# Kernel optimization log

Hardware: AMD Instinct MI355X
Metric: run time of the kernel (lower is better)

The kernel has to match this reference:

```python
import jax, jax.numpy as jnp
import numpy as np

EMBED = 256; G = 8; NC = 6; NL = 4; NP = 13
BS = 1; NA = 900
IMG_W, IMG_H = 704.0, 256.0
LEVEL_HW = [(64, 176), (32, 88), (16, 44), (8, 22)]


def setup_inputs() -> dict:
    key = jax.random.key(0)
    ks = jax.random.split(key, 12)
    inp = {}
    inp["instance_feature"] = jax.random.normal(ks[0], (BS, NA, EMBED), jnp.float32)
    inp["anchor_embed"] = jax.random.normal(ks[1], (BS, NA, EMBED), jnp.float32)
    # key points in normalized [0,1) cube; projection matrix maps them to pixel coords
    inp["key_points"] = jax.random.uniform(ks[2], (BS, NA, NP, 3), jnp.float32)
    for i, (h, w) in enumerate(LEVEL_HW):
        inp[f"fm{i}"] = jax.random.normal(ks[3 + i], (BS, NC, EMBED, h, w), jnp.float32)
    # intrinsics-like projection: x->x*W, y->y*H, depth ~ z+0.5, plus per-camera jitter
    base = jnp.array([[IMG_W, 0.0, 0.0, 0.0],
                      [0.0, IMG_H, 0.0, 0.0],
                      [0.0, 0.0, 1.0, 0.5],
                      [0.0, 0.0, 0.0, 1.0]], jnp.float32)
    inp["projection_mat"] = base[None, None] + 0.05 * jax.random.normal(ks[7], (BS, NC, 4, 4), jnp.float32)
    inp["image_wh"] = jnp.broadcast_to(jnp.array([IMG_W, IMG_H], jnp.float32), (BS, NC, 2))
    inp["w_weights"] = 0.02 * jax.random.normal(ks[8], (EMBED, G * NC * NL * NP), jnp.float32)
    inp["b_weights"] = jnp.zeros((G * NC * NL * NP,), jnp.float32)
    inp["w_out"] = 0.02 * jax.random.normal(ks[9], (EMBED, EMBED), jnp.float32)
    inp["b_out"] = jnp.zeros((EMBED,), jnp.float32)
    return inp


def _grid_sample(fm, grid):
    # fm: (B, C, H, W); grid: (B, A, P, 2) in [-1,1]. Bilinear, zero padding,
    # align_corners=False (torch F.grid_sample defaults). Returns (B, A, P, C).
    B, C, H, W = fm.shape
    A, P = grid.shape[1], grid.shape[2]
    gx = (grid[..., 0] + 1.0) * (W * 0.5) - 0.5
    gy = (grid[..., 1] + 1.0) * (H * 0.5) - 0.5
    x0 = jnp.floor(gx); y0 = jnp.floor(gy)
    fmf = jnp.transpose(fm.reshape(B, C, H * W), (0, 2, 1))  # (B, HW, C)

    def gather(xi, yi):
        valid = (xi >= 0) & (xi <= W - 1) & (yi >= 0) & (yi <= H - 1)
        xc = jnp.clip(xi, 0, W - 1).astype(jnp.int32)
        yc = jnp.clip(yi, 0, H - 1).astype(jnp.int32)
        idx = (yc * W + xc).reshape(B, A * P, 1)
        g = jnp.take_along_axis(fmf, idx, axis=1).reshape(B, A, P, C)
        return g * valid[..., None].astype(fm.dtype)

    wx1 = gx - x0; wx0 = 1.0 - wx1
    wy1 = gy - y0; wy0 = 1.0 - wy1
    return (gather(x0, y0) * (wx0 * wy0)[..., None]
            + gather(x0 + 1.0, y0) * (wx1 * wy0)[..., None]
            + gather(x0, y0 + 1.0) * (wx0 * wy1)[..., None]
            + gather(x0 + 1.0, y0 + 1.0) * (wx1 * wy1)[..., None])


def reference(instance_feature, anchor_embed, key_points, fm0, fm1, fm2, fm3,
              projection_mat, image_wh, w_weights, b_weights, w_out, b_out):
    bs, na = instance_feature.shape[:2]
    gd = EMBED // G
    # _get_weights: softmax over (cams*levels*pts) jointly, per group
    feat = instance_feature + anchor_embed
    w = (feat @ w_weights + b_weights).reshape(bs, na, NC * NL * NP, G)
    w = jax.nn.softmax(w, axis=2).reshape(bs, na, NC, NL, NP, G)
    # feature_sampling: project 3D key points to each camera's pixel plane
    kp_h = jnp.concatenate([key_points, jnp.ones_like(key_points[..., :1])], axis=-1)
    p2 = jnp.einsum('bcij,banj->bcani', projection_mat, kp_h)  # (bs,cams,na,pts,4)
    xy = p2[..., :2] / jnp.maximum(p2[..., 2:3], 1e-5)
    grid = (xy / image_wh[:, :, None, None]) * 2.0 - 1.0
    grid = grid.reshape(bs * NC, na, NP, 2)
    # bilinear sample every pyramid level for every camera
    feats = jnp.stack([
        _grid_sample(fm.reshape(bs * NC, EMBED, fm.shape[-2], fm.shape[-1]), grid)
        for fm in (fm0, fm1, fm2, fm3)
    ], axis=0)  # (L, bs*cams, na, pts, E)
    feats = feats.reshape(NL, bs, NC, na, NP, G, gd)
    # multi_view_level_fusion: weighted sum over cams and levels, per group
    fused = jnp.einsum('baclpg,lbcapgd->bapgd', w, feats).reshape(bs, na, NP, EMBED)
    out = fused.sum(axis=2)  # sum over key points
    return out @ w_out + b_out + instance_feature  # output_proj + residual 'add'
```

## Files before the change

kernel.cpp:

```cpp
#include <hip/hip_runtime.h>
#include <hip/hip_bf16.h>
#include <hip/hip_fp16.h>
#include <cstdint>

#define EMBED 256
#define GPS 8
#define NCAM 6
#define NLVL 4
#define NPT 13
#define NANC 900
#define NSAMP (NCAM*NLVL*NPT)
#define NWCOL (GPS*NSAMP)
#define MPAD 928
#define WSTRIDE 328

typedef __attribute__((ext_vector_type(8))) short bf16x8;
typedef __attribute__((ext_vector_type(16))) float f32x16;
typedef __attribute__((ext_vector_type(8))) unsigned short ushort8_t;

__device__ __forceinline__ ushort bf16bits(float x) {
    __hip_bfloat16 h = __float2bfloat16(x);
    return *reinterpret_cast<ushort*>(&h);
}
__device__ __forceinline__ ushort h16bits(float x) {
    __half h = __float2half(x);
    return *reinterpret_cast<ushort*>(&h);
}
__device__ __forceinline__ __half2 u2h2(unsigned u) {
    union { unsigned u; __half2 h; } cv; cv.u = u; return cv.h;
}

__global__ __launch_bounds__(256) void k_prep(
        const float* __restrict__ fm0, const float* __restrict__ fm1,
        const float* __restrict__ fm2, const float* __restrict__ fm3,
        __half* __restrict__ t0, __half* __restrict__ t1,
        __half* __restrict__ t2, __half* __restrict__ t3,
        const float* __restrict__ wlin, __hip_bfloat16* __restrict__ wt,
        const float* __restrict__ inst, const float* __restrict__ anch,
        __hip_bfloat16* __restrict__ featB,
        const float* __restrict__ kp, const float* __restrict__ proj,
        float* __restrict__ pxy) {
    __shared__ ushort lds2[256 * 64];
    int b = blockIdx.x;
    int t = threadIdx.x;
    if (b < 1404) {
        const float* in; __half* outp; int HW, chunks, lb;
        if (b < 1056)      { in = fm0; outp = t0; HW = 11264; chunks = 176; lb = b; }
        else if (b < 1320) { in = fm1; outp = t1; HW = 2816;  chunks = 44;  lb = b - 1056; }
        else if (b < 1386) { in = fm2; outp = t2; HW = 704;   chunks = 11;  lb = b - 1320; }
        else               { in = fm3; outp = t3; HW = 176;   chunks = 3;   lb = b - 1386; }
        int c = lb / chunks;
        int hw0 = (lb - c * chunks) * 64;
        int q = t & 15, eg = t >> 4;
        bool vld = (hw0 + q * 4 + 3) < HW;
        const float* srcq = in + (size_t)c * EMBED * HW + hw0 + q * 4;
        float4 vals[16];
        #pragma unroll
        for (int r = 0; r < 16; r++) {
            int e = eg + r * 16;
            vals[r] = vld ? *(const float4*)(srcq + (size_t)e * HW)
                          : make_float4(0.f, 0.f, 0.f, 0.f);
        }
        #pragma unroll
        for (int r = 0; r < 16; r++) {
            int e = eg + r * 16;
            int sw = ((e >> 3) & 15) * 4;
            ushort4 u;
            u.x = h16bits(vals[r].x); u.y = h16bits(vals[r].y);
            u.z = h16bits(vals[r].z); u.w = h16bits(vals[r].w);
            *reinterpret_cast<ushort4*>(&lds2[e * 64 + ((q * 4) ^ sw)]) = u;
        }
        __syncthreads();
        ushort* outb = reinterpret_cast<ushort*>(outp) + ((size_t)c * HW + hw0) * EMBED;
        #pragma unroll
        for (int r = 0; r < 8; r++) {
            int flat = r * 2048 + t * 8;
            int hw = flat >> 8;
            int e0 = flat & 255;
            if (hw0 + hw < HW) {
                ushort8_t u;
                #pragma unroll
                for (int j = 0; j < 8; j++) {
                    int e = e0 + j;
                    int sw = ((e >> 3) & 15) * 4;
                    u[j] = lds2[e * 64 + (hw ^ sw)];
                }
                *reinterpret_cast<ushort8_t*>(outb + flat) = u;
            }
        }
    } else if (b < 1560) {
        int b1 = b - 1404;
        int kt = b1 / 39, nt = b1 - kt * 39;
        int k0 = kt * 64, n0 = nt * 64;
        int grp = t >> 6, nn = t & 63;
        #pragma unroll
        for (int r = 0; r < 16; r++) {
            int kk = grp * 16 + r;
            lds2[kk * 65 + nn] = bf16bits(wlin[(size_t)(k0 + kk) * NWCOL + n0 + nn]);
        }
        __syncthreads();
        ushort* wtb = reinterpret_cast<ushort*>(wt);
        int kk2 = t & 63;
        #pragma unroll
        for (int r = 0; r < 16; r++) {
            int nn2 = grp * 16 + r;
            wtb[(size_t)(n0 + nn2) * EMBED + k0 + kk2] = lds2[kk2 * 65 + nn2];
        }
    } else if (b < 1785) {
        int base = (b - 1560) * 1024 + t * 4;
        float4 a = *(const float4*)&inst[base];
        float4 c = *(const float4*)&anch[base];
        ushort4 r;
        r.x = bf16bits(a.x + c.x); r.y = bf16bits(a.y + c.y);
        r.z = bf16bits(a.z + c.z); r.w = bf16bits(a.w + c.w);
        *reinterpret_cast<ushort4*>(reinterpret_cast<ushort*>(featB) + base) = r;
    } else if (b < 1792) {
        int base = 900 * EMBED + (b - 1785) * 1024 + t * 4;
        ushort4 z; z.x = z.y = z.z = z.w = 0;
        *reinterpret_cast<ushort4*>(reinterpret_cast<ushort*>(featB) + base) = z;
    } else {
        int i = (b - 1792) * 256 + t;
        if (i < NANC * NCAM * NPT) {
            int a = i / (NCAM * NPT);
            int r = i - a * (NCAM * NPT);
            int c = r / NPT;
            int p = r - c * NPT;
            const float* M = proj + c * 16;
            const float* k3 = kp + ((size_t)a * NPT + p) * 3;
            float kx = k3[0], ky = k3[1], kz = k3[2];
            float X = M[0] * kx + M[1] * ky + M[2] * kz + M[3];
            float Y = M[4] * kx + M[5] * ky + M[6] * kz + M[7];
            float Z = M[8] * kx + M[9] * ky + M[10] * kz + M[11];
            float invz = 1.f / fmaxf(Z, 1e-5f);
            pxy[(size_t)i * 2 + 0] = X * invz;
            pxy[(size_t)i * 2 + 1] = Y * invz;
        }
    }
}

#define MT 29
#define NT 78
__global__ __launch_bounds__(256) void k_gemm(const __hip_bfloat16* __restrict__ featB,
                                              const __hip_bfloat16* __restrict__ wt,
                                              const float* __restrict__ blin,
                                              float* __restrict__ logits) {
    int wv = threadIdx.x >> 6, lane = threadIdx.x & 63;
    int idx = blockIdx.x * 4 + wv;
    if (idx >= MT * NT) return;
    int mt = idx % MT, nt = idx / MT;
    int m0 = mt * 32, n0 = nt * 32;
    int l31 = lane & 31;
    int khalf = (lane >> 5) * 8;
    const short* ap = reinterpret_cast<const short*>(featB) + (size_t)(m0 + l31) * EMBED + khalf;
    const short* bp = reinterpret_cast<const short*>(wt)    + (size_t)(n0 + l31) * EMBED + khalf;
    f32x16 acc = {};
    #pragma unroll 8
    for (int ki = 0; ki < 16; ki++) {
        bf16x8 a = *reinterpret_cast<const bf16x8*>(ap + ki * 16);
        bf16x8 bb = *reinterpret_cast<const bf16x8*>(bp + ki * 16);
        acc = __builtin_amdgcn_mfma_f32_32x32x16_bf16(a, bb, acc, 0, 0, 0);
    }
    float bias = blin[n0 + l31];
    int colg = n0 + l31;
    #pragma unroll
    for (int r = 0; r < 16; r++) {
        int row = (r & 3) + 8 * (r >> 2) + 4 * (lane >> 5);
        int grow = m0 + row;
        if (grow < NANC)
            logits[(size_t)grow * NWCOL + colg] = acc[r] + bias;
    }
}

__global__ __launch_bounds__(512) void k_aggregate(const __half* __restrict__ f0,
                                                   const __half* __restrict__ f1,
                                                   const __half* __restrict__ f2,
                                                   const __half* __restrict__ f3,
                                                   const float* __restrict__ logits,
                                                   const float* __restrict__ pxy,
                                                   const float* __restrict__ wout,
                                                   const float* __restrict__ bout,
                                                   const float* __restrict__ inst,
                                                   float* __restrict__ out) {
    __shared__ float wT[GPS * WSTRIDE];
    __shared__ float xyS[NCAM * NPT * 2];
    __shared__ float redS[8][EMBED];
    __shared__ float pS[EMBED];
    int a = blockIdx.x;
    int tid = threadIdx.x;
    for (int j = tid; j < NWCOL; j += 512)
        wT[(j & 7) * WSTRIDE + (j >> 3)] = logits[(size_t)a * NWCOL + j];
    for (int j = tid; j < NCAM * NPT * 2; j += 512)
        xyS[j] = pxy[(size_t)a * NCAM * NPT * 2 + j];
    __syncthreads();
    int wave = tid >> 6;
    int lane = tid & 63;
    {
        int g = wave;
        float m = -1e30f;
        for (int s = lane; s < NSAMP; s += 64) m = fmaxf(m, wT[g * WSTRIDE + s]);
        #pragma unroll
        for (int off = 32; off; off >>= 1) m = fmaxf(m, __shfl_xor(m, off));
        float ssum = 0.f;
        for (int s = lane; s < NSAMP; s += 64) ssum += __expf(wT[g * WSTRIDE + s] - m);
        #pragma unroll
        for (int off = 32; off; off >>= 1) ssum += __shfl_xor(ssum, off);
        float rs = 1.f / ssum;
        for (int s = lane; s < NSAMP; s += 64)
            wT[g * WSTRIDE + s] = __expf(wT[g * WSTRIDE + s] - m) * rs;
    }
    __syncthreads();
    int e0 = lane * 4;
    int g = lane >> 3;
    float a0 = 0.f, a1 = 0.f, a2 = 0.f, a3 = 0.f;
    const __half* fms[4] = { f0, f1, f2, f3 };
    const int Wl_[4] = { 176, 88, 44, 22 };
    const int Hl_[4] = { 64, 32, 16, 8 };
    #pragma unroll
    for (int l = 0; l < 4; l++) {
        const int Wl = Wl_[l], Hl = Hl_[l];
        const int HWl = Wl * Hl;
        const float scale = 0.25f / (float)(1 << l);
        const __half* fm = fms[l];
        for (int cp = wave; cp < NCAM * NPT; cp += 8) {
            float X = xyS[cp * 2], Y = xyS[cp * 2 + 1];
            float gx = fmaf(X, scale, -0.5f);
            float gy = fmaf(Y, scale, -0.5f);
            float x0f = floorf(gx), y0f = floorf(gy);
            float fx = gx - x0f, fy = gy - y0f;
            int x0 = (int)x0f, y0 = (int)y0f;
            int x1 = x0 + 1, y1 = y0 + 1;
            bool vx0 = (x0 >= 0) && (x0 < Wl);
            bool vx1 = (x1 >= 0) && (x1 < Wl);
            bool vy0 = (y0 >= 0) && (y0 < Hl);
            bool vy1 = (y1 >= 0) && (y1 < Hl);
            float w00 = (vx0 && vy0) ? (1.f - fx) * (1.f - fy) : 0.f;
            float w01 = (vx1 && vy0) ? fx * (1.f - fy) : 0.f;
            float w10 = (vx0 && vy1) ? (1.f - fx) * fy : 0.f;
            float w11 = (vx1 && vy1) ? fx * fy : 0.f;
            if (w00 + w01 + w10 + w11 == 0.f) continue;
            int c = cp / NPT, p = cp - c * NPT;
            int xc0 = min(max(x0, 0), Wl - 1), xc1 = min(max(x1, 0), Wl - 1);
            int yc0 = min(max(y0, 0), Hl - 1), yc1 = min(max(y1, 0), Hl - 1);
            const __half* base = fm + (size_t)c * HWl * EMBED + e0;
            uint2 u00 = *(const uint2*)(base + (size_t)(yc0 * Wl + xc0) * EMBED);
            uint2 u01 = *(const uint2*)(base + (size_t)(yc0 * Wl + xc1) * EMBED);
            uint2 u10 = *(const uint2*)(base + (size_t)(yc1 * Wl + xc0) * EMBED);
            uint2 u11 = *(const uint2*)(base + (size_t)(yc1 * Wl + xc1) * EMBED);
            __half2 W00 = __float2half2_rn(w00), W01 = __float2half2_rn(w01);
            __half2 W10 = __float2half2_rn(w10), W11 = __float2half2_rn(w11);
            __half2 blo = __hfma2(u2h2(u00.x), W00,
                          __hfma2(u2h2(u01.x), W01,
                          __hfma2(u2h2(u10.x), W10,
                          __hmul2(u2h2(u11.x), W11))));
            __half2 bhi = __hfma2(u2h2(u00.y), W00,
                          __hfma2(u2h2(u01.y), W01,
                          __hfma2(u2h2(u10.y), W10,
                          __hmul2(u2h2(u11.y), W11))));
            float2 flo = __half22float2(blo);
            float2 fhi = __half22float2(bhi);
            float wg = wT[g * WSTRIDE + (c * NLVL + l) * NPT + p];
            a0 = fmaf(wg, flo.x, a0);
            a1 = fmaf(wg, flo.y, a1);
            a2 = fmaf(wg, fhi.x, a2);
            a3 = fmaf(wg, fhi.y, a3);
        }
    }
    redS[wave][e0 + 0] = a0; redS[wave][e0 + 1] = a1;
    redS[wave][e0 + 2] = a2; redS[wave][e0 + 3] = a3;
    __syncthreads();
    int col = tid & 255;
    int kh = tid >> 8;
    if (kh == 0) {
        float s = redS[0][col] + redS[1][col] + redS[2][col] + redS[3][col]
                + redS[4][col] + redS[5][col] + redS[6][col] + redS[7][col];
        redS[0][col] = s;
    }
    __syncthreads();
    float acc = 0.f;
    int kbase = kh * 128;
    #pragma unroll 8
    for (int k = 0; k < 128; k++)
        acc = fmaf(redS[0][kbase + k], wout[(size_t)(kbase + k) * EMBED + col], acc);
    if (kh == 1) pS[col] = acc;
    __syncthreads();
    if (kh == 0)
        out[(size_t)a * EMBED + col] = acc + pS[col] + bout[col] + inst[(size_t)a * EMBED + col];
}

extern "C" void kernel_launch(void* const* d_in, const int* in_sizes, int n_in,
                              void* d_out, int out_size, void* d_ws, size_t ws_size,
                              hipStream_t stream) {
    const float* inst = (const float*)d_in[0];
    const float* anch = (const float*)d_in[1];
    const float* kp   = (const float*)d_in[2];
    const float* fm0  = (const float*)d_in[3];
    const float* fm1  = (const float*)d_in[4];
    const float* fm2  = (const float*)d_in[5];
    const float* fm3  = (const float*)d_in[6];
    const float* proj = (const float*)d_in[7];
    const float* wlin = (const float*)d_in[9];
    const float* blin = (const float*)d_in[10];
    const float* wout = (const float*)d_in[11];
    const float* bout = (const float*)d_in[12];
    float* out = (float*)d_out;

    char* ws = (char*)d_ws;
    size_t off = 0;
    auto alloc = [&](size_t bytes) -> void* {
        void* p = ws + off;
        off = (off + bytes + 255) & ~(size_t)255;
        return p;
    };
    __half* t0 = (__half*)alloc((size_t)NCAM * 11264 * EMBED * 2);
    __half* t1 = (__half*)alloc((size_t)NCAM * 2816 * EMBED * 2);
    __half* t2 = (__half*)alloc((size_t)NCAM * 704 * EMBED * 2);
    __half* t3 = (__half*)alloc((size_t)NCAM * 176 * EMBED * 2);
    __hip_bfloat16* wt    = (__hip_bfloat16*)alloc((size_t)NWCOL * EMBED * 2);
    __hip_bfloat16* featB = (__hip_bfloat16*)alloc((size_t)MPAD * EMBED * 2);
    float* logits = (float*)alloc((size_t)NANC * NWCOL * 4);
    float* pxy    = (float*)alloc((size_t)NANC * NCAM * NPT * 2 * 4);

    k_prep<<<dim3(2067), 256, 0, stream>>>(fm0, fm1, fm2, fm3, t0, t1, t2, t3,
                                           wlin, wt, inst, anch, featB, kp, proj, pxy);
    k_gemm<<<dim3((MT * NT + 3) / 4), 256, 0, stream>>>(featB, wt, blin, logits);
    k_aggregate<<<dim3(NANC), 512, 0, stream>>>(t0, t1, t2, t3, logits, pxy,
                                                wout, bout, inst, out);
}
```

Before: 221.5 us.

## Compact valid bilinear samples into shared list and software-pipeline gathers

The aggregate kernel now computes bilinear corner offsets and weights for all 312 samples in parallel, one per thread. Only samples with nonzero weight are compacted into a shared-memory list using ballot and an atomic counter. The eight waves then split the compacted list evenly and double-buffer the four corner loads, so the next sample's gathers are in flight while the current one accumulates. This removes divergent per-wave skipping, balances load across waves and hides gather latency. The cost is extra shared memory and sync points, plus a single contiguous feature buffer addressed by 32-bit offsets.

```diff
diff --git a/kernel.cpp b/kernel.cpp
--- a/kernel.cpp
+++ b/kernel.cpp
@@ -13,6 +13,13 @@
 #define NWCOL (GPS*NSAMP)
 #define MPAD 928
 #define WSTRIDE 328
+#define MAXENT 320
+
+#define FMOFF0 0
+#define FMOFF1 17301504
+#define FMOFF2 21626880
+#define FMOFF3 22708224
+#define TALL_ELEMS 22978560
 
 typedef __attribute__((ext_vector_type(8))) short bf16x8;
 typedef __attribute__((ext_vector_type(16))) float f32x16;
@@ -171,10 +178,7 @@
     }
 }
 
-__global__ __launch_bounds__(512) void k_aggregate(const __half* __restrict__ f0,
-                                                   const __half* __restrict__ f1,
-                                                   const __half* __restrict__ f2,
-                                                   const __half* __restrict__ f3,
+__global__ __launch_bounds__(512) void k_aggregate(const __half* __restrict__ tAll,
                                                    const float* __restrict__ logits,
                                                    const float* __restrict__ pxy,
                                                    const float* __restrict__ wout,
@@ -185,15 +189,20 @@
     __shared__ float xyS[NCAM * NPT * 2];
     __shared__ float redS[8][EMBED];
     __shared__ float pS[EMBED];
+    __shared__ int4  eOff[MAXENT];
+    __shared__ float4 eW[MAXENT];
+    __shared__ int   eS[MAXENT];
+    __shared__ int   cntS;
     int a = blockIdx.x;
     int tid = threadIdx.x;
+    int wave = tid >> 6;
+    int lane = tid & 63;
+    if (tid == 0) cntS = 0;
     for (int j = tid; j < NWCOL; j += 512)
         wT[(j & 7) * WSTRIDE + (j >> 3)] = logits[(size_t)a * NWCOL + j];
     for (int j = tid; j < NCAM * NPT * 2; j += 512)
         xyS[j] = pxy[(size_t)a * NCAM * NPT * 2 + j];
     __syncthreads();
-    int wave = tid >> 6;
-    int lane = tid & 63;
     {
         int g = wave;
         float m = -1e30f;
@@ -208,21 +217,14 @@
         for (int s = lane; s < NSAMP; s += 64)
             wT[g * WSTRIDE + s] = __expf(wT[g * WSTRIDE + s] - m) * rs;
     }
-    __syncthreads();
-    int e0 = lane * 4;
-    int g = lane >> 3;
-    float a0 = 0.f, a1 = 0.f, a2 = 0.f, a3 = 0.f;
-    const __half* fms[4] = { f0, f1, f2, f3 };
-    const int Wl_[4] = { 176, 88, 44, 22 };
-    const int Hl_[4] = { 64, 32, 16, 8 };
-    #pragma unroll
-    for (int l = 0; l < 4; l++) {
-        const int Wl = Wl_[l], Hl = Hl_[l];
-        const int HWl = Wl * Hl;
-        const float scale = 0.25f / (float)(1 << l);
-        const __half* fm = fms[l];
-        for (int cp = wave; cp < NCAM * NPT; cp += 8) {
-            float X = xyS[cp * 2], Y = xyS[cp * 2 + 1];
+    {
+        bool valid = false; int4 o4; float4 w4;
+        if (tid < NSAMP) {
+            int c = tid / 52, rem = tid - c * 52;
+            int l = rem / 13, p = rem - l * 13;
+            float X = xyS[(c * NPT + p) * 2], Y = xyS[(c * NPT + p) * 2 + 1];
+            int Wl = 176 >> l, Hl = 64 >> l;
+            float scale = 0.25f / (float)(1 << l);
             float gx = fmaf(X, scale, -0.5f);
             float gy = fmaf(Y, scale, -0.5f);
             float x0f = floorf(gx), y0f = floorf(gy);
@@ -233,36 +235,90 @@
             bool vx1 = (x1 >= 0) && (x1 < Wl);
             bool vy0 = (y0 >= 0) && (y0 < Hl);
             bool vy1 = (y1 >= 0) && (y1 < Hl);
-            float w00 = (vx0 && vy0) ? (1.f - fx) * (1.f - fy) : 0.f;
-            float w01 = (vx1 && vy0) ? fx * (1.f - fy) : 0.f;
-            float w10 = (vx0 && vy1) ? (1.f - fx) * fy : 0.f;
-            float w11 = (vx1 && vy1) ? fx * fy : 0.f;
-            if (w00 + w01 + w10 + w11 == 0.f) continue;
-            int c = cp / NPT, p = cp - c * NPT;
-            int xc0 = min(max(x0, 0), Wl - 1), xc1 = min(max(x1, 0), Wl - 1);
-            int yc0 = min(max(y0, 0), Hl - 1), yc1 = min(max(y1, 0), Hl - 1);
-            const __half* base = fm + (size_t)c * HWl * EMBED + e0;
-            uint2 u00 = *(const uint2*)(base + (size_t)(yc0 * Wl + xc0) * EMBED);
-            uint2 u01 = *(const uint2*)(base + (size_t)(yc0 * Wl + xc1) * EMBED);
-            uint2 u10 = *(const uint2*)(base + (size_t)(yc1 * Wl + xc0) * EMBED);
-            uint2 u11 = *(const uint2*)(base + (size_t)(yc1 * Wl + xc1) * EMBED);
-            __half2 W00 = __float2half2_rn(w00), W01 = __float2half2_rn(w01);
-            __half2 W10 = __float2half2_rn(w10), W11 = __float2half2_rn(w11);
-            __half2 blo = __hfma2(u2h2(u00.x), W00,
-                          __hfma2(u2h2(u01.x), W01,
-                          __hfma2(u2h2(u10.x), W10,
-                          __hmul2(u2h2(u11.x), W11))));
-            __half2 bhi = __hfma2(u2h2(u00.y), W00,
-                          __hfma2(u2h2(u01.y), W01,
-                          __hfma2(u2h2(u10.y), W10,
-                          __hmul2(u2h2(u11.y), W11))));
-            float2 flo = __half22float2(blo);
-            float2 fhi = __half22float2(bhi);
-            float wg = wT[g * WSTRIDE + (c * NLVL + l) * NPT + p];
-            a0 = fmaf(wg, flo.x, a0);
-            a1 = fmaf(wg, flo.y, a1);
-            a2 = fmaf(wg, fhi.x, a2);
-            a3 = fmaf(wg, fhi.y, a3);
+            w4.x = (vx0 && vy0) ? (1.f - fx) * (1.f - fy) : 0.f;
+            w4.y = (vx1 && vy0) ? fx * (1.f - fy) : 0.f;
+            w4.z = (vx0 && vy1) ? (1.f - fx) * fy : 0.f;
+            w4.w = (vx1 && vy1) ? fx * fy : 0.f;
+            if (w4.x + w4.y + w4.z + w4.w > 0.f) {
+                valid = true;
+                int xc0 = min(max(x0, 0), Wl - 1), xc1 = min(max(x1, 0), Wl - 1);
+                int yc0 = min(max(y0, 0), Hl - 1), yc1 = min(max(y1, 0), Hl - 1);
+                const int lvlBase[4] = { FMOFF0, FMOFF1, FMOFF2, FMOFF3 };
+                int cb = lvlBase[l] + c * (Wl * Hl) * EMBED;
+                o4.x = cb + (yc0 * Wl + xc0) * EMBED;
+                o4.y = cb + (yc0 * Wl + xc1) * EMBED;
+                o4.z = cb + (yc1 * Wl + xc0) * EMBED;
+                o4.w = cb + (yc1 * Wl + xc1) * EMBED;
+            }
+        }
+        unsigned long long mask = __ballot(valid);
+        int prefix = __popcll(mask & ((1ull << lane) - 1ull));
+        int wcount = __popcll(mask);
+        int basev = 0;
+        if (lane == 0 && wcount) basev = atomicAdd(&cntS, wcount);
+        basev = __shfl(basev, 0);
+        if (valid) {
+            int pos = basev + prefix;
+            eOff[pos] = o4; eW[pos] = w4; eS[pos] = tid;
+        }
+    }
+    __syncthreads();
+    int cnt = cntS;
+    int cnt_pad = (cnt + 15) & ~15;
+    for (int j = cnt + tid; j < cnt_pad; j += 512) {
+        eOff[j] = make_int4(0, 0, 0, 0);
+        eW[j] = make_float4(0.f, 0.f, 0.f, 0.f);
+        eS[j] = 0;
+    }
+    __syncthreads();
+    int e0 = lane * 4;
+    int g = lane >> 3;
+    float a0 = 0.f, a1 = 0.f, a2 = 0.f, a3 = 0.f;
+    auto consume = [&](const float4& w, int sIdx,
+                       uint2 l0, uint2 l1, uint2 l2, uint2 l3) {
+        float wg = wT[g * WSTRIDE + sIdx];
+        __half2 W00 = __float2half2_rn(w.x), W01 = __float2half2_rn(w.y);
+        __half2 W10 = __float2half2_rn(w.z), W11 = __float2half2_rn(w.w);
+        __half2 blo = __hfma2(u2h2(l0.x), W00,
+                      __hfma2(u2h2(l1.x), W01,
+                      __hfma2(u2h2(l2.x), W10,
+                      __hmul2(u2h2(l3.x), W11))));
+        __half2 bhi = __hfma2(u2h2(l0.y), W00,
+                      __hfma2(u2h2(l1.y), W01,
+                      __hfma2(u2h2(l2.y), W10,
+                      __hmul2(u2h2(l3.y), W11))));
+        float2 flo = __half22float2(blo);
+        float2 fhi = __half22float2(bhi);
+        a0 = fmaf(wg, flo.x, a0);
+        a1 = fmaf(wg, flo.y, a1);
+        a2 = fmaf(wg, fhi.x, a2);
+        a3 = fmaf(wg, fhi.y, a3);
+    };
+    int per = cnt_pad >> 3;
+    if (per > 0) {
+        int idx = wave;
+        int4 oA = eOff[idx]; float4 wA = eW[idx]; int sA = eS[idx];
+        uint2 vA0 = *(const uint2*)(tAll + oA.x + e0);
+        uint2 vA1 = *(const uint2*)(tAll + oA.y + e0);
+        uint2 vA2 = *(const uint2*)(tAll + oA.z + e0);
+        uint2 vA3 = *(const uint2*)(tAll + oA.w + e0);
+        for (int it = 0; it < per; it += 2) {
+            int j = idx + 8;
+            int4 oB = eOff[j]; float4 wB = eW[j]; int sB = eS[j];
+            uint2 vB0 = *(const uint2*)(tAll + oB.x + e0);
+            uint2 vB1 = *(const uint2*)(tAll + oB.y + e0);
+            uint2 vB2 = *(const uint2*)(tAll + oB.z + e0);
+            uint2 vB3 = *(const uint2*)(tAll + oB.w + e0);
+            consume(wA, sA, vA0, vA1, vA2, vA3);
+            idx = j + 8;
+            if (it + 2 < per) {
+                oA = eOff[idx]; wA = eW[idx]; sA = eS[idx];
+                vA0 = *(const uint2*)(tAll + oA.x + e0);
+                vA1 = *(const uint2*)(tAll + oA.y + e0);
+                vA2 = *(const uint2*)(tAll + oA.z + e0);
+                vA3 = *(const uint2*)(tAll + oA.w + e0);
+            }
+            consume(wB, sB, vB0, vB1, vB2, vB3);
         }
     }
     redS[wave][e0 + 0] = a0; redS[wave][e0 + 1] = a1;
@@ -311,10 +367,11 @@
         off = (off + bytes + 255) & ~(size_t)255;
         return p;
     };
-    __half* t0 = (__half*)alloc((size_t)NCAM * 11264 * EMBED * 2);
-    __half* t1 = (__half*)alloc((size_t)NCAM * 2816 * EMBED * 2);
-    __half* t2 = (__half*)alloc((size_t)NCAM * 704 * EMBED * 2);
-    __half* t3 = (__half*)alloc((size_t)NCAM * 176 * EMBED * 2);
+    __half* tAll = (__half*)alloc((size_t)TALL_ELEMS * 2);
+    __half* t0 = tAll + FMOFF0;
+    __half* t1 = tAll + FMOFF1;
+    __half* t2 = tAll + FMOFF2;
+    __half* t3 = tAll + FMOFF3;
     __hip_bfloat16* wt    = (__hip_bfloat16*)alloc((size_t)NWCOL * EMBED * 2);
     __hip_bfloat16* featB = (__hip_bfloat16*)alloc((size_t)MPAD * EMBED * 2);
     float* logits = (float*)alloc((size_t)NANC * NWCOL * 4);
@@ -323,6 +380,6 @@
     k_prep<<<dim3(2067), 256, 0, stream>>>(fm0, fm1, fm2, fm3, t0, t1, t2, t3,
                                            wlin, wt, inst, anch, featB, kp, proj, pxy);
     k_gemm<<<dim3((MT * NT + 3) / 4), 256, 0, stream>>>(featB, wt, blin, logits);
-    k_aggregate<<<dim3(NANC), 512, 0, stream>>>(t0, t1, t2, t3, logits, pxy,
+    k_aggregate<<<dim3(NANC), 512, 0, stream>>>(tAll, logits, pxy,
                                                 wout, bout, inst, out);
 }
```

Result: faster. 217.1 us (-2.0%).
